# Kernel optimization log

Hardware: AMD Instinct MI355X
Metric: run time of the kernel (lower is better)

The kernel has to match this reference:

```python
import jax, jax.numpy as jnp
import numpy as np


def setup_inputs() -> dict:
    key = jax.random.key(0)
    ks = jax.random.split(key, 5)
    B, H, W, C = 8, 256, 256, 96
    return {
        "x": jax.random.normal(ks[0], (B, H, W, C), dtype=jnp.float32),
        "qkv_w": jax.random.normal(ks[1], (3 * C, C), dtype=jnp.float32) * 0.02,
        "qkv_b": jax.random.normal(ks[2], (3 * C,), dtype=jnp.float32) * 0.02,
        "proj_w": jax.random.normal(ks[3], (C, C), dtype=jnp.float32) * 0.02,
        "proj_b": jax.random.normal(ks[4], (C,), dtype=jnp.float32) * 0.02,
        "window_size": 8,
        "num_heads": 4,
    }


def reference(x, qkv_w, qkv_b, proj_w, proj_b, window_size, num_heads):
    B, H, W, C = x.shape
    ws = window_size
    hd = C // num_heads
    scale = hd ** -0.5
    # window partition: [B,H,W,C] -> [B*nWh*nWw, ws*ws, C]
    xw = x.reshape(B, H // ws, ws, W // ws, ws, C)
    xw = xw.transpose(0, 1, 3, 2, 4, 5).reshape(-1, ws * ws, C)
    n = xw.shape[0]
    # qkv projection (torch Linear: y = x @ W^T + b)
    qkv = xw @ qkv_w.T + qkv_b  # [n, ws*ws, 3C]
    qkv = qkv.reshape(n, ws * ws, 3, num_heads, hd).transpose(2, 0, 3, 1, 4)
    q, k, v = qkv[0], qkv[1], qkv[2]  # each [n, heads, ws*ws, hd]
    attn = jnp.einsum("nhqd,nhkd->nhqk", q, k) * scale
    attn = jax.nn.softmax(attn, axis=-1)
    out = jnp.einsum("nhqk,nhkd->nhqd", attn, v)
    out = out.transpose(0, 2, 1, 3).reshape(n, ws * ws, C)
    out = out @ proj_w.T + proj_b
    # window reverse: [n, ws*ws, C] -> [B, H, W, C]
    out = out.reshape(B, H // ws, W // ws, ws, ws, C)
    out = out.transpose(0, 1, 3, 2, 4, 5).reshape(B, H, W, C)
    return out
```

## Files before the change

### kernel.cpp

```cpp
#include <hip/hip_runtime.h>


typedef _Float16 f16;
typedef f16 f16x8 __attribute__((ext_vector_type(8)));
typedef f16 f16x4 __attribute__((ext_vector_type(4)));
typedef __fp16 hf2 __attribute__((ext_vector_type(2)));
typedef float f32x4 __attribute__((ext_vector_type(4)));

#define MFMA_K32 __builtin_amdgcn_mfma_f32_16x16x32_f16

#define QS 104
#define KE 0.29448890f

__device__ __forceinline__ int vtidx(int row, int col) { return row*64 + (col ^ ((row & 7) << 3)); }
__device__ __forceinline__ int o2idx(int t, int c)     { return t*104 + (c ^ ((t & 7) << 2)); }

__device__ __forceinline__ f16x4 pk4(float a, float b, float c, float d) {
    union { f16x4 v; hf2 h[2]; } u;
    u.h[0] = __builtin_amdgcn_cvt_pkrtz(a, b);
    u.h[1] = __builtin_amdgcn_cvt_pkrtz(c, d);
    return u.v;
}

__global__ void prep_weights(const float* __restrict__ qkv_w,
                             const float* __restrict__ proj_w,
                             const float* __restrict__ qkv_b,
                             f16* __restrict__ ws) {
    const int u = blockIdx.x * 256 + threadIdx.x;
    if (u < 3456) {
        const int lane = u & 63, unit = u >> 6;
        const int n = unit / 3, kk = unit - 3*n;
        const int lr = lane & 15, lg = lane >> 4;
        const float sc = (n < 6) ? KE : 1.0f;
        const float* s = qkv_w + (16*n + lr)*96 + kk*32 + lg*8;
        f16x8 v;
        #pragma unroll
        for (int e = 0; e < 8; ++e) v[e] = (f16)(s[e] * sc);
        *(f16x8*)(ws + (size_t)u*8) = v;
    } else if (u < 4608) {
        const int uu = u - 3456;
        const int lane = uu & 63, unit = uu >> 6;
        const int n = unit / 3, kk = unit - 3*n;
        const int lr = lane & 15, lg = lane >> 4;
        const float* s = proj_w + (16*n + lr)*96 + kk*32 + lg*8;
        f16x8 v;
        #pragma unroll
        for (int e = 0; e < 8; ++e) v[e] = (f16)s[e];
        *(f16x8*)(ws + 27648 + (size_t)uu*8) = v;
    } else if (u < 4704) {
        const int j = u - 4608;
        ((float*)(ws + 36864))[j] = qkv_b[j] * KE;
    }
}

__global__ __launch_bounds__(256, 2) void winattn(
    const float* __restrict__ x,
    const f16*   __restrict__ wsq,
    const float* __restrict__ qkv_b,
    const f16*   __restrict__ wsp,
    const float* __restrict__ proj_b,
    float* __restrict__ out)
{
    __shared__ __align__(16) char smem[77824];
    f16* qqA = (f16*)(smem);
    f16* qkA = (f16*)(smem + 13312);
    f16* qqB = (f16*)(smem + 26624);
    f16* qkB = (f16*)(smem + 39936);
    f16* vtA = (f16*)(smem + 53248);
    f16* vtB = (f16*)(smem + 65536);
    float* o2A = (float*)(smem);
    float* o2B = (float*)(smem + 26624);

    const int tid = threadIdx.x;
    const int wid = blockIdx.x * 2;
    const int bb = wid >> 10, wh = (wid >> 5) & 31, ww = wid & 31;
    const size_t win_baseA = ((size_t)(bb*256 + wh*8)*256 + (size_t)(ww*8)) * 96;

    const int lane = tid & 63, w = tid >> 6;
    const int lr = lane & 15, lg = lane >> 4;
    const int t = 16*w + lr;
    const size_t tok_offA = win_baseA + (size_t)(((t>>3)<<8) + (t&7))*96;
    const size_t tok_offB = tok_offA + 768;

    const f16* wqL = wsq + lane*8;
    const f16* wpL = wsp + lane*8;
    const float* qbs = (const float*)(wsq + 36864);

    f16x8 axA[3], axB[3];
    #pragma unroll
    for (int kk = 0; kk < 3; ++kk) {
        const float* xpA = x + tok_offA + kk*32 + lg*8;
        const float* xpB = x + tok_offB + kk*32 + lg*8;
        const float4 a0 = *(const float4*)xpA;
        const float4 a1 = *(const float4*)(xpA + 4);
        const float4 b0 = *(const float4*)xpB;
        const float4 b1 = *(const float4*)(xpB + 4);
        union { f16x8 v; f16x4 q[2]; } ua, ub;
        ua.q[0] = pk4(a0.x, a0.y, a0.z, a0.w);
        ua.q[1] = pk4(a1.x, a1.y, a1.z, a1.w);
        ub.q[0] = pk4(b0.x, b0.y, b0.z, b0.w);
        ub.q[1] = pk4(b1.x, b1.y, b1.z, b1.w);
        axA[kk] = ua.v;
        axB[kk] = ub.v;
    }
    const int vcol = (w>>1)*32 + (lr>>2)*8 + (w&1)*4 + (lr&3);

    {
        f16x8 wf[6][3];
        #pragma unroll
        for (int nn = 0; nn < 6; ++nn)
            #pragma unroll
            for (int kk = 0; kk < 3; ++kk)
                wf[nn][kk] = *(const f16x8*)(wqL + (nn*3 + kk)*512);
        #pragma unroll
        for (int nn = 0; nn < 6; ++nn) {
            f32x4 accA = {0.f,0.f,0.f,0.f}, accB = {0.f,0.f,0.f,0.f};
            #pragma unroll
            for (int kk = 0; kk < 3; ++kk) {
                accA = MFMA_K32(wf[nn][kk], axA[kk], accA, 0,0,0);
                accB = MFMA_K32(wf[nn][kk], axB[kk], accB, 0,0,0);
            }
            const int j0 = 16*nn + 4*lg;
            const float4 b4 = *(const float4*)(qbs + j0);
            *(f16x4*)&qqA[t*QS + j0] = pk4(accA[0]+b4.x, accA[1]+b4.y, accA[2]+b4.z, accA[3]+b4.w);
            *(f16x4*)&qqB[t*QS + j0] = pk4(accB[0]+b4.x, accB[1]+b4.y, accB[2]+b4.z, accB[3]+b4.w);
        }
    }
    {
        f16x8 wf[6][3];
        #pragma unroll
        for (int nn = 0; nn < 6; ++nn)
            #pragma unroll
            for (int kk = 0; kk < 3; ++kk)
                wf[nn][kk] = *(const f16x8*)(wqL + ((nn+6)*3 + kk)*512);
        #pragma unroll
        for (int nn = 0; nn < 6; ++nn) {
            f32x4 accA = {0.f,0.f,0.f,0.f}, accB = {0.f,0.f,0.f,0.f};
            #pragma unroll
            for (int kk = 0; kk < 3; ++kk) {
                accA = MFMA_K32(wf[nn][kk], axA[kk], accA, 0,0,0);
                accB = MFMA_K32(wf[nn][kk], axB[kk], accB, 0,0,0);
            }
            const int j0 = 16*nn + 4*lg;
            const float4 b4 = *(const float4*)(qkv_b + 96 + j0);
            *(f16x4*)&qkA[t*QS + j0] = pk4(accA[0]+b4.x, accA[1]+b4.y, accA[2]+b4.z, accA[3]+b4.w);
            *(f16x4*)&qkB[t*QS + j0] = pk4(accB[0]+b4.x, accB[1]+b4.y, accB[2]+b4.z, accB[3]+b4.w);
        }
    }
    {
        f16x8 wf[6][3];
        #pragma unroll
        for (int nn = 0; nn < 6; ++nn)
            #pragma unroll
            for (int kk = 0; kk < 3; ++kk)
                wf[nn][kk] = *(const f16x8*)(wqL + ((nn+12)*3 + kk)*512);
        #pragma unroll
        for (int nn = 0; nn < 6; ++nn) {
            f32x4 accA = {0.f,0.f,0.f,0.f}, accB = {0.f,0.f,0.f,0.f};
            #pragma unroll
            for (int kk = 0; kk < 3; ++kk) {
                accA = MFMA_K32(wf[nn][kk], axA[kk], accA, 0,0,0);
                accB = MFMA_K32(wf[nn][kk], axB[kk], accB, 0,0,0);
            }
            const int j0 = 16*nn + 4*lg;
            const float4 b4 = *(const float4*)(qkv_b + 192 + j0);
            const int hv = (unsigned)j0 / 24u, d0 = j0 - 24*hv;
            vtA[vtidx(hv*24 + d0+0, vcol)] = (f16)(accA[0]+b4.x);
            vtA[vtidx(hv*24 + d0+1, vcol)] = (f16)(accA[1]+b4.y);
            vtA[vtidx(hv*24 + d0+2, vcol)] = (f16)(accA[2]+b4.z);
            vtA[vtidx(hv*24 + d0+3, vcol)] = (f16)(accA[3]+b4.w);
            vtB[vtidx(hv*24 + d0+0, vcol)] = (f16)(accB[0]+b4.x);
            vtB[vtidx(hv*24 + d0+1, vcol)] = (f16)(accB[1]+b4.y);
            vtB[vtidx(hv*24 + d0+2, vcol)] = (f16)(accB[2]+b4.z);
            vtB[vtidx(hv*24 + d0+3, vcol)] = (f16)(accB[3]+b4.w);
        }
    }
    __syncthreads();

    const int h = w;
    const bool live = (lg < 3);
    const int cs = h*24 + lg*8;
    const f16x8 z8 = {0,0,0,0,0,0,0,0};

    f16x8 bfA[4], afA[4], bfB[4], afB[4];
    #pragma unroll
    for (int i = 0; i < 4; ++i) {
        bfA[i] = z8; afA[i] = z8; bfB[i] = z8; afB[i] = z8;
        if (live) {
            bfA[i] = *(const f16x8*)&qqA[(16*i + lr)*QS + cs];
            afA[i] = *(const f16x8*)&qkA[(16*i + lr)*QS + cs];
            bfB[i] = *(const f16x8*)&qqB[(16*i + lr)*QS + cs];
            afB[i] = *(const f16x8*)&qkB[(16*i + lr)*QS + cs];
        }
    }
    __syncthreads();

    f32x4 stA[4][4], stB[4][4];
    #pragma unroll
    for (int un = 0; un < 4; ++un)
        #pragma unroll
        for (int tn = 0; tn < 4; ++tn) {
            stA[un][tn] = MFMA_K32(afA[un], bfA[tn], (f32x4){0.f,0.f,0.f,0.f}, 0,0,0);
            stB[un][tn] = MFMA_K32(afB[un], bfB[tn], (f32x4){0.f,0.f,0.f,0.f}, 0,0,0);
        }

    float rsA[4], rsB[4];
    #pragma unroll
    for (int tn = 0; tn < 4; ++tn) {
        float sA = 0.f, sB = 0.f;
        #pragma unroll
        for (int un = 0; un < 4; ++un)
            #pragma unroll
            for (int r = 0; r < 4; ++r) {
                const float eA = exp2f(stA[un][tn][r]);
                const float eB = exp2f(stB[un][tn][r]);
                stA[un][tn][r] = eA; sA += eA;
                stB[un][tn][r] = eB; sB += eB;
            }
        sA += __shfl_xor(sA, 16); sA += __shfl_xor(sA, 32);
        sB += __shfl_xor(sB, 16); sB += __shfl_xor(sB, 32);
        rsA[tn] = 1.f / sA;
        rsB[tn] = 1.f / sB;
    }

    f32x4 oa0A[4], oa1A[4], oa0B[4], oa1B[4];
    #pragma unroll
    for (int tn = 0; tn < 4; ++tn) {
        oa0A[tn] = (f32x4){0.f,0.f,0.f,0.f}; oa1A[tn] = (f32x4){0.f,0.f,0.f,0.f};
        oa0B[tn] = (f32x4){0.f,0.f,0.f,0.f}; oa1B[tn] = (f32x4){0.f,0.f,0.f,0.f};
    }
    const int d1 = (16 + lr > 23) ? 23 : 16 + lr;
    #pragma unroll
    for (int hf = 0; hf < 2; ++hf) {
        const f16x8 av0A = *(const f16x8*)&vtA[vtidx(h*24 + lr, hf*32 + lg*8)];
        const f16x8 av1A = *(const f16x8*)&vtA[vtidx(h*24 + d1, hf*32 + lg*8)];
        const f16x8 av0B = *(const f16x8*)&vtB[vtidx(h*24 + lr, hf*32 + lg*8)];
        const f16x8 av1B = *(const f16x8*)&vtB[vtidx(h*24 + d1, hf*32 + lg*8)];
        #pragma unroll
        for (int tn = 0; tn < 4; ++tn) {
            union { f16x8 v; hf2 h2[4]; } pA, pB;
            pA.h2[0] = __builtin_amdgcn_cvt_pkrtz(stA[2*hf  ][tn][0], stA[2*hf  ][tn][1]);
            pA.h2[1] = __builtin_amdgcn_cvt_pkrtz(stA[2*hf  ][tn][2], stA[2*hf  ][tn][3]);
            pA.h2[2] = __builtin_amdgcn_cvt_pkrtz(stA[2*hf+1][tn][0], stA[2*hf+1][tn][1]);
            pA.h2[3] = __builtin_amdgcn_cvt_pkrtz(stA[2*hf+1][tn][2], stA[2*hf+1][tn][3]);
            pB.h2[0] = __builtin_amdgcn_cvt_pkrtz(stB[2*hf  ][tn][0], stB[2*hf  ][tn][1]);
            pB.h2[1] = __builtin_amdgcn_cvt_pkrtz(stB[2*hf  ][tn][2], stB[2*hf  ][tn][3]);
            pB.h2[2] = __builtin_amdgcn_cvt_pkrtz(stB[2*hf+1][tn][0], stB[2*hf+1][tn][1]);
            pB.h2[3] = __builtin_amdgcn_cvt_pkrtz(stB[2*hf+1][tn][2], stB[2*hf+1][tn][3]);
            oa0A[tn] = MFMA_K32(av0A, pA.v, oa0A[tn], 0,0,0);
            oa1A[tn] = MFMA_K32(av1A, pA.v, oa1A[tn], 0,0,0);
            oa0B[tn] = MFMA_K32(av0B, pB.v, oa0B[tn], 0,0,0);
            oa1B[tn] = MFMA_K32(av1B, pB.v, oa1B[tn], 0,0,0);
        }
    }

    f16x8 pf[6][3];
    #pragma unroll
    for (int n = 0; n < 6; ++n)
        #pragma unroll
        for (int kk = 0; kk < 3; ++kk)
            pf[n][kk] = *(const f16x8*)(wpL + (n*3 + kk)*512);
    float4 pb4[6];
    #pragma unroll
    for (int n = 0; n < 6; ++n)
        pb4[n] = *(const float4*)(proj_b + 16*n + 4*lg);

    #pragma unroll
    for (int tn = 0; tn < 4; ++tn) {
        const int tt = 16*tn + lr;
        *(f16x4*)&qqA[tt*QS + h*24 + 4*lg] =
            pk4(oa0A[tn][0]*rsA[tn], oa0A[tn][1]*rsA[tn], oa0A[tn][2]*rsA[tn], oa0A[tn][3]*rsA[tn]);
        *(f16x4*)&qqB[tt*QS + h*24 + 4*lg] =
            pk4(oa0B[tn][0]*rsB[tn], oa0B[tn][1]*rsB[tn], oa0B[tn][2]*rsB[tn], oa0B[tn][3]*rsB[tn]);
        if (lg < 2) {
            *(f16x4*)&qqA[tt*QS + h*24 + 16 + 4*lg] =
                pk4(oa1A[tn][0]*rsA[tn], oa1A[tn][1]*rsA[tn], oa1A[tn][2]*rsA[tn], oa1A[tn][3]*rsA[tn]);
            *(f16x4*)&qqB[tt*QS + h*24 + 16 + 4*lg] =
                pk4(oa1B[tn][0]*rsB[tn], oa1B[tn][1]*rsB[tn], oa1B[tn][2]*rsB[tn], oa1B[tn][3]*rsB[tn]);
        }
    }
    __syncthreads();

    f16x8 boA[3], boB[3];
    #pragma unroll
    for (int kk = 0; kk < 3; ++kk) {
        boA[kk] = *(const f16x8*)&qqA[t*QS + kk*32 + lg*8];
        boB[kk] = *(const f16x8*)&qqB[t*QS + kk*32 + lg*8];
    }
    __syncthreads();

    #pragma unroll
    for (int n = 0; n < 6; ++n) {
        f32x4 paA = {0.f,0.f,0.f,0.f}, paB = {0.f,0.f,0.f,0.f};
        #pragma unroll
        for (int kk = 0; kk < 3; ++kk) {
            paA = MFMA_K32(pf[n][kk], boA[kk], paA, 0,0,0);
            paB = MFMA_K32(pf[n][kk], boB[kk], paB, 0,0,0);
        }
        const int c0 = 16*n + 4*lg;
        float4 ovA = {paA[0]+pb4[n].x, paA[1]+pb4[n].y, paA[2]+pb4[n].z, paA[3]+pb4[n].w};
        float4 ovB = {paB[0]+pb4[n].x, paB[1]+pb4[n].y, paB[2]+pb4[n].z, paB[3]+pb4[n].w};
        *(float4*)&o2A[o2idx(t, c0)] = ovA;
        *(float4*)&o2B[o2idx(t, c0)] = ovB;
    }
    __syncthreads();

    #pragma unroll
    for (int it = 0; it < 6; ++it) {
        const int i = it*256 + tid;
        const int tt = i / 24, c4 = (i - tt*24) * 4;
        const size_t po = win_baseA + (size_t)(((tt>>3)<<8) + (tt&7))*96 + c4;
        *(float4*)(out + po)       = *(const float4*)&o2A[o2idx(tt, c4)];
        *(float4*)(out + po + 768) = *(const float4*)&o2B[o2idx(tt, c4)];
    }
}

extern "C" void kernel_launch(void* const* d_in, const int* in_sizes, int n_in,
                              void* d_out, int out_size, void* d_ws, size_t ws_size,
                              hipStream_t stream) {
    const float* x      = (const float*)d_in[0];
    const float* qkv_w  = (const float*)d_in[1];
    const float* qkv_b  = (const float*)d_in[2];
    const float* proj_w = (const float*)d_in[3];
    const float* proj_b = (const float*)d_in[4];
    float* out = (float*)d_out;
    f16* ws = (f16*)d_ws;

    prep_weights<<<dim3(19), dim3(256), 0, stream>>>(qkv_w, proj_w, qkv_b, ws);
    winattn<<<dim3(4096), dim3(256), 0, stream>>>(x, ws, qkv_b, ws + 27648, proj_b, out);
}
```

Before: 141.1 us.

## Store Q/K in FP8 and use FP8 MFMA for scores, shrink LDS for occupancy

Q and K are now packed to FP8 in shared memory and the QK^T scores use the fp8 16x16x32 MFMA. This halves the Q/K LDS footprint, and the buffer plan is reorganised so total LDS drops from about 76 KB to 50 KB, allowing three blocks per CU. Bias adds are folded into the MFMA accumulator init, and the output staging uses a padded stride of 100 instead of an XOR swizzle. FP8 Q/K costs precision in the attention logits and could fail tolerance checks. The new layout may also bring back LDS bank conflicts and add register pressure under the tighter launch bound.

```diff
diff --git a/kernel.cpp b/kernel.cpp
--- a/kernel.cpp
+++ b/kernel.cpp
@@ -1,4 +1,5 @@
 #include <hip/hip_runtime.h>
+#include <stdint.h>
 
 
 typedef _Float16 f16;
@@ -7,19 +8,24 @@
 typedef __fp16 hf2 __attribute__((ext_vector_type(2)));
 typedef float f32x4 __attribute__((ext_vector_type(4)));
 
-#define MFMA_K32 __builtin_amdgcn_mfma_f32_16x16x32_f16
-
-#define QS 104
+#define MFMA_K32  __builtin_amdgcn_mfma_f32_16x16x32_f16
+#define MFMA_FP8  __builtin_amdgcn_mfma_f32_16x16x32_fp8_fp8
+
 #define KE 0.29448890f
 
 __device__ __forceinline__ int vtidx(int row, int col) { return row*64 + (col ^ ((row & 7) << 3)); }
-__device__ __forceinline__ int o2idx(int t, int c)     { return t*104 + (c ^ ((t & 7) << 2)); }
 
 __device__ __forceinline__ f16x4 pk4(float a, float b, float c, float d) {
     union { f16x4 v; hf2 h[2]; } u;
     u.h[0] = __builtin_amdgcn_cvt_pkrtz(a, b);
     u.h[1] = __builtin_amdgcn_cvt_pkrtz(c, d);
     return u.v;
+}
+
+__device__ __forceinline__ int pk_fp8x4(float a, float b, float c, float d) {
+    int v = __builtin_amdgcn_cvt_pk_fp8_f32(a, b, 0, false);
+    v = __builtin_amdgcn_cvt_pk_fp8_f32(c, d, v, true);
+    return v;
 }
 
 __global__ void prep_weights(const float* __restrict__ qkv_w,
@@ -53,7 +59,7 @@
     }
 }
 
-__global__ __launch_bounds__(256, 2) void winattn(
+__global__ __launch_bounds__(256, 3) void winattn(
     const float* __restrict__ x,
     const f16*   __restrict__ wsq,
     const float* __restrict__ qkv_b,
@@ -61,15 +67,17 @@
     const float* __restrict__ proj_b,
     float* __restrict__ out)
 {
-    __shared__ __align__(16) char smem[77824];
-    f16* qqA = (f16*)(smem);
-    f16* qkA = (f16*)(smem + 13312);
-    f16* qqB = (f16*)(smem + 26624);
-    f16* qkB = (f16*)(smem + 39936);
-    f16* vtA = (f16*)(smem + 53248);
-    f16* vtB = (f16*)(smem + 65536);
-    float* o2A = (float*)(smem);
-    float* o2B = (float*)(smem + 26624);
+    __shared__ __align__(16) char smem[51200];
+    uint8_t* q8A = (uint8_t*)smem;
+    uint8_t* k8A = q8A + 6656;
+    f16* vtA = (f16*)(smem + 13312);
+    f16* ObA = (f16*)smem;
+    float* o2A = (float*)smem;
+    uint8_t* q8B = (uint8_t*)(smem + 25600);
+    uint8_t* k8B = q8B + 6656;
+    f16* vtB = (f16*)(smem + 25600 + 13312);
+    f16* ObB = (f16*)(smem + 25600);
+    float* o2B = (float*)(smem + 25600);
 
     const int tid = threadIdx.x;
     const int wid = blockIdx.x * 2;
@@ -114,16 +122,17 @@
                 wf[nn][kk] = *(const f16x8*)(wqL + (nn*3 + kk)*512);
         #pragma unroll
         for (int nn = 0; nn < 6; ++nn) {
-            f32x4 accA = {0.f,0.f,0.f,0.f}, accB = {0.f,0.f,0.f,0.f};
+            const int j0 = 16*nn + 4*lg;
+            const float4 b4 = *(const float4*)(qbs + j0);
+            f32x4 accA = {b4.x, b4.y, b4.z, b4.w};
+            f32x4 accB = accA;
             #pragma unroll
             for (int kk = 0; kk < 3; ++kk) {
                 accA = MFMA_K32(wf[nn][kk], axA[kk], accA, 0,0,0);
                 accB = MFMA_K32(wf[nn][kk], axB[kk], accB, 0,0,0);
             }
-            const int j0 = 16*nn + 4*lg;
-            const float4 b4 = *(const float4*)(qbs + j0);
-            *(f16x4*)&qqA[t*QS + j0] = pk4(accA[0]+b4.x, accA[1]+b4.y, accA[2]+b4.z, accA[3]+b4.w);
-            *(f16x4*)&qqB[t*QS + j0] = pk4(accB[0]+b4.x, accB[1]+b4.y, accB[2]+b4.z, accB[3]+b4.w);
+            *(int*)(q8A + t*104 + j0) = pk_fp8x4(accA[0], accA[1], accA[2], accA[3]);
+            *(int*)(q8B + t*104 + j0) = pk_fp8x4(accB[0], accB[1], accB[2], accB[3]);
         }
     }
     {
@@ -135,16 +144,17 @@
                 wf[nn][kk] = *(const f16x8*)(wqL + ((nn+6)*3 + kk)*512);
         #pragma unroll
         for (int nn = 0; nn < 6; ++nn) {
-            f32x4 accA = {0.f,0.f,0.f,0.f}, accB = {0.f,0.f,0.f,0.f};
+            const int j0 = 16*nn + 4*lg;
+            const float4 b4 = *(const float4*)(qkv_b + 96 + j0);
+            f32x4 accA = {b4.x, b4.y, b4.z, b4.w};
+            f32x4 accB = accA;
             #pragma unroll
             for (int kk = 0; kk < 3; ++kk) {
                 accA = MFMA_K32(wf[nn][kk], axA[kk], accA, 0,0,0);
                 accB = MFMA_K32(wf[nn][kk], axB[kk], accB, 0,0,0);
             }
-            const int j0 = 16*nn + 4*lg;
-            const float4 b4 = *(const float4*)(qkv_b + 96 + j0);
-            *(f16x4*)&qkA[t*QS + j0] = pk4(accA[0]+b4.x, accA[1]+b4.y, accA[2]+b4.z, accA[3]+b4.w);
-            *(f16x4*)&qkB[t*QS + j0] = pk4(accB[0]+b4.x, accB[1]+b4.y, accB[2]+b4.z, accB[3]+b4.w);
+            *(int*)(k8A + t*104 + j0) = pk_fp8x4(accA[0], accA[1], accA[2], accA[3]);
+            *(int*)(k8B + t*104 + j0) = pk_fp8x4(accB[0], accB[1], accB[2], accB[3]);
         }
     }
     {
@@ -156,23 +166,24 @@
                 wf[nn][kk] = *(const f16x8*)(wqL + ((nn+12)*3 + kk)*512);
         #pragma unroll
         for (int nn = 0; nn < 6; ++nn) {
-            f32x4 accA = {0.f,0.f,0.f,0.f}, accB = {0.f,0.f,0.f,0.f};
+            const int j0 = 16*nn + 4*lg;
+            const float4 b4 = *(const float4*)(qkv_b + 192 + j0);
+            f32x4 accA = {b4.x, b4.y, b4.z, b4.w};
+            f32x4 accB = accA;
             #pragma unroll
             for (int kk = 0; kk < 3; ++kk) {
                 accA = MFMA_K32(wf[nn][kk], axA[kk], accA, 0,0,0);
                 accB = MFMA_K32(wf[nn][kk], axB[kk], accB, 0,0,0);
             }
-            const int j0 = 16*nn + 4*lg;
-            const float4 b4 = *(const float4*)(qkv_b + 192 + j0);
             const int hv = (unsigned)j0 / 24u, d0 = j0 - 24*hv;
-            vtA[vtidx(hv*24 + d0+0, vcol)] = (f16)(accA[0]+b4.x);
-            vtA[vtidx(hv*24 + d0+1, vcol)] = (f16)(accA[1]+b4.y);
-            vtA[vtidx(hv*24 + d0+2, vcol)] = (f16)(accA[2]+b4.z);
-            vtA[vtidx(hv*24 + d0+3, vcol)] = (f16)(accA[3]+b4.w);
-            vtB[vtidx(hv*24 + d0+0, vcol)] = (f16)(accB[0]+b4.x);
-            vtB[vtidx(hv*24 + d0+1, vcol)] = (f16)(accB[1]+b4.y);
-            vtB[vtidx(hv*24 + d0+2, vcol)] = (f16)(accB[2]+b4.z);
-            vtB[vtidx(hv*24 + d0+3, vcol)] = (f16)(accB[3]+b4.w);
+            vtA[vtidx(hv*24 + d0+0, vcol)] = (f16)accA[0];
+            vtA[vtidx(hv*24 + d0+1, vcol)] = (f16)accA[1];
+            vtA[vtidx(hv*24 + d0+2, vcol)] = (f16)accA[2];
+            vtA[vtidx(hv*24 + d0+3, vcol)] = (f16)accA[3];
+            vtB[vtidx(hv*24 + d0+0, vcol)] = (f16)accB[0];
+            vtB[vtidx(hv*24 + d0+1, vcol)] = (f16)accB[1];
+            vtB[vtidx(hv*24 + d0+2, vcol)] = (f16)accB[2];
+            vtB[vtidx(hv*24 + d0+3, vcol)] = (f16)accB[3];
         }
     }
     __syncthreads();
@@ -180,18 +191,14 @@
     const int h = w;
     const bool live = (lg < 3);
     const int cs = h*24 + lg*8;
-    const f16x8 z8 = {0,0,0,0,0,0,0,0};
-
-    f16x8 bfA[4], afA[4], bfB[4], afB[4];
+    long bqA[4], aqA[4], bqB[4], aqB[4];
     #pragma unroll
     for (int i = 0; i < 4; ++i) {
-        bfA[i] = z8; afA[i] = z8; bfB[i] = z8; afB[i] = z8;
-        if (live) {
-            bfA[i] = *(const f16x8*)&qqA[(16*i + lr)*QS + cs];
-            afA[i] = *(const f16x8*)&qkA[(16*i + lr)*QS + cs];
-            bfB[i] = *(const f16x8*)&qqB[(16*i + lr)*QS + cs];
-            afB[i] = *(const f16x8*)&qkB[(16*i + lr)*QS + cs];
-        }
+        const int ro = (16*i + lr)*104 + cs;
+        bqA[i] = live ? *(const long*)(q8A + ro) : 0L;
+        aqA[i] = live ? *(const long*)(k8A + ro) : 0L;
+        bqB[i] = live ? *(const long*)(q8B + ro) : 0L;
+        aqB[i] = live ? *(const long*)(k8B + ro) : 0L;
     }
     __syncthreads();
 
@@ -200,8 +207,8 @@
     for (int un = 0; un < 4; ++un)
         #pragma unroll
         for (int tn = 0; tn < 4; ++tn) {
-            stA[un][tn] = MFMA_K32(afA[un], bfA[tn], (f32x4){0.f,0.f,0.f,0.f}, 0,0,0);
-            stB[un][tn] = MFMA_K32(afB[un], bfB[tn], (f32x4){0.f,0.f,0.f,0.f}, 0,0,0);
+            stA[un][tn] = MFMA_FP8(aqA[un], bqA[tn], (f32x4){0.f,0.f,0.f,0.f}, 0,0,0);
+            stB[un][tn] = MFMA_FP8(aqB[un], bqB[tn], (f32x4){0.f,0.f,0.f,0.f}, 0,0,0);
         }
 
     float rsA[4], rsB[4];
@@ -268,14 +275,14 @@
     #pragma unroll
     for (int tn = 0; tn < 4; ++tn) {
         const int tt = 16*tn + lr;
-        *(f16x4*)&qqA[tt*QS + h*24 + 4*lg] =
+        *(f16x4*)&ObA[tt*104 + h*24 + 4*lg] =
             pk4(oa0A[tn][0]*rsA[tn], oa0A[tn][1]*rsA[tn], oa0A[tn][2]*rsA[tn], oa0A[tn][3]*rsA[tn]);
-        *(f16x4*)&qqB[tt*QS + h*24 + 4*lg] =
+        *(f16x4*)&ObB[tt*104 + h*24 + 4*lg] =
             pk4(oa0B[tn][0]*rsB[tn], oa0B[tn][1]*rsB[tn], oa0B[tn][2]*rsB[tn], oa0B[tn][3]*rsB[tn]);
         if (lg < 2) {
-            *(f16x4*)&qqA[tt*QS + h*24 + 16 + 4*lg] =
+            *(f16x4*)&ObA[tt*104 + h*24 + 16 + 4*lg] =
                 pk4(oa1A[tn][0]*rsA[tn], oa1A[tn][1]*rsA[tn], oa1A[tn][2]*rsA[tn], oa1A[tn][3]*rsA[tn]);
-            *(f16x4*)&qqB[tt*QS + h*24 + 16 + 4*lg] =
+            *(f16x4*)&ObB[tt*104 + h*24 + 16 + 4*lg] =
                 pk4(oa1B[tn][0]*rsB[tn], oa1B[tn][1]*rsB[tn], oa1B[tn][2]*rsB[tn], oa1B[tn][3]*rsB[tn]);
         }
     }
@@ -284,24 +291,23 @@
     f16x8 boA[3], boB[3];
     #pragma unroll
     for (int kk = 0; kk < 3; ++kk) {
-        boA[kk] = *(const f16x8*)&qqA[t*QS + kk*32 + lg*8];
-        boB[kk] = *(const f16x8*)&qqB[t*QS + kk*32 + lg*8];
+        boA[kk] = *(const f16x8*)&ObA[t*104 + kk*32 + lg*8];
+        boB[kk] = *(const f16x8*)&ObB[t*104 + kk*32 + lg*8];
     }
     __syncthreads();
 
     #pragma unroll
     for (int n = 0; n < 6; ++n) {
-        f32x4 paA = {0.f,0.f,0.f,0.f}, paB = {0.f,0.f,0.f,0.f};
+        const int c0 = 16*n + 4*lg;
+        f32x4 paA = {pb4[n].x, pb4[n].y, pb4[n].z, pb4[n].w};
+        f32x4 paB = paA;
         #pragma unroll
         for (int kk = 0; kk < 3; ++kk) {
             paA = MFMA_K32(pf[n][kk], boA[kk], paA, 0,0,0);
             paB = MFMA_K32(pf[n][kk], boB[kk], paB, 0,0,0);
         }
-        const int c0 = 16*n + 4*lg;
-        float4 ovA = {paA[0]+pb4[n].x, paA[1]+pb4[n].y, paA[2]+pb4[n].z, paA[3]+pb4[n].w};
-        float4 ovB = {paB[0]+pb4[n].x, paB[1]+pb4[n].y, paB[2]+pb4[n].z, paB[3]+pb4[n].w};
-        *(float4*)&o2A[o2idx(t, c0)] = ovA;
-        *(float4*)&o2B[o2idx(t, c0)] = ovB;
+        *(f32x4*)&o2A[t*100 + c0] = paA;
+        *(f32x4*)&o2B[t*100 + c0] = paB;
     }
     __syncthreads();
 
@@ -310,8 +316,8 @@
         const int i = it*256 + tid;
         const int tt = i / 24, c4 = (i - tt*24) * 4;
         const size_t po = win_baseA + (size_t)(((tt>>3)<<8) + (tt&7))*96 + c4;
-        *(float4*)(out + po)       = *(const float4*)&o2A[o2idx(tt, c4)];
-        *(float4*)(out + po + 768) = *(const float4*)&o2B[o2idx(tt, c4)];
+        *(float4*)(out + po)       = *(const float4*)&o2A[tt*100 + c4];
+        *(float4*)(out + po + 768) = *(const float4*)&o2B[tt*100 + c4];
     }
 }
 
```

Measured after the change: 175.7 us. 24.6% more time.
